# Performance work log

Hardware: AMD Instinct MI355X
Metric: run time of the kernel (lower is better)

The kernel has to match this reference:

```python
import jax, jax.numpy as jnp
import numpy as np

N_CELLS, C_N, K, D_N = 128, 256, 16, 64
G, HS, HM, HMOD, HEADS = 8, 128, 128, 64, 4


def setup_inputs() -> dict:
    key = jax.random.key(0)
    ks = list(jax.random.split(key, 12))
    rng = np.random.default_rng(0)
    # top-K neighbors per neuron within each cell, self excluded, sorted (as in __init__)
    scores = rng.random((N_CELLS, C_N, C_N), dtype=np.float32)
    scores[:, np.arange(C_N), np.arange(C_N)] = -np.inf
    topk = np.argpartition(-scores, K, axis=-1)[..., :K]
    conn_idx = jnp.asarray(np.sort(topk, axis=-1).astype(np.int32))
    cell_to_group = jnp.asarray((np.arange(N_CELLS) % G).astype(np.int32))

    def nrm(k, shape, scale):
        return jax.random.normal(k, shape, dtype=jnp.float32) * scale

    inp = {
        'h': nrm(ks[0], (N_CELLS, C_N, D_N), 1.0),
        'neuron_id': nrm(ks[1], (N_CELLS, C_N, D_N), 0.02),
        'neuron_key': nrm(ks[2], (N_CELLS, C_N, D_N), 0.02),
        'state_w1': nrm(ks[3], (HS, 2 * D_N), (2.0 / (2 * D_N)) ** 0.5),
        'state_b1': jnp.zeros((HS,), jnp.float32),
        'state_gs1': jnp.ones((G, HS), jnp.float32),
        'state_gb1': jnp.zeros((G, HS), jnp.float32),
        'state_w2': nrm(ks[4], (D_N, HS), 0.1 * (2.0 / HS) ** 0.5),
        'state_b2': jnp.zeros((D_N,), jnp.float32),
        'state_gs2': jnp.ones((G, D_N), jnp.float32),
        'state_gb2': jnp.zeros((G, D_N), jnp.float32),
        'msg_w1': nrm(ks[5], (HM, 2 * D_N), (2.0 / (2 * D_N)) ** 0.5),
        'msg_b1': jnp.zeros((HM,), jnp.float32),
        'msg_gs1': jnp.ones((G, HM), jnp.float32),
        'msg_gb1': jnp.zeros((G, HM), jnp.float32),
        'msg_w2': nrm(ks[6], (D_N, HM), 0.1 * (2.0 / HM) ** 0.5),
        'msg_b2': jnp.zeros((D_N,), jnp.float32),
        'msg_gs2': jnp.ones((G, D_N), jnp.float32),
        'msg_gb2': jnp.zeros((G, D_N), jnp.float32),
        'mod_w1': nrm(ks[7], (N_CELLS, D_N, HMOD), (2.0 / D_N) ** 0.5),
        'mod_b1': jnp.zeros((N_CELLS, HMOD), jnp.float32),
        'mod_w2': nrm(ks[8], (N_CELLS, HMOD, D_N), 0.01 * (2.0 / HMOD) ** 0.5),
        'mod_b2': jnp.zeros((N_CELLS, D_N), jnp.float32),
        'conn_idx': conn_idx,
        'cell_to_group': cell_to_group,
    }
    return inp


def reference(h, neuron_id, neuron_key,
              state_w1, state_b1, state_gs1, state_gb1,
              state_w2, state_b2, state_gs2, state_gb2,
              msg_w1, msg_b1, msg_gs1, msg_gb1,
              msg_w2, msg_b2, msg_gs2, msg_gb2,
              mod_w1, mod_b1, mod_w2, mod_b2,
              conn_idx, cell_to_group):
    g = cell_to_group  # [N]
    dh = D_N // HEADS
    gather = jax.vmap(lambda per_cell, idx: per_cell[idx])  # [C,D],[C,K] -> [C,K,D]

    nbr = gather(h, conn_idx)          # [N,C,K,D] neighbor states
    kid = gather(neuron_id, conn_idx)  # [N,C,K,D] neighbor identity vectors

    # multi-head attention weights over the K neighbors
    q = neuron_key.reshape(N_CELLS, C_N, HEADS, dh)
    kk = kid.reshape(N_CELLS, C_N, K, HEADS, dh)
    logits = jnp.einsum('nchd,nckhd->nckh', q, kk) / (dh ** 0.5)
    attn = jax.nn.softmax(logits, axis=2)  # softmax over K

    # per-edge message MLP with per-group gain/bias
    x = jnp.concatenate([nbr, jnp.broadcast_to(h[:, :, None, :], nbr.shape)], axis=-1)  # [N,C,K,2D]
    m1 = jax.nn.gelu(jnp.einsum('nckf,hf->nckh', x, msg_w1) + msg_b1)
    m1 = m1 * msg_gs1[g][:, None, None, :] + msg_gb1[g][:, None, None, :]
    m2 = jnp.einsum('nckh,dh->nckd', m1, msg_w2) + msg_b2
    m2 = m2 * msg_gs2[g][:, None, None, :] + msg_gb2[g][:, None, None, :]

    # attention-weighted aggregation over neighbors
    m2h = m2.reshape(N_CELLS, C_N, K, HEADS, dh)
    agg = jnp.einsum('nckh,nckhd->nchd', attn, m2h).reshape(N_CELLS, C_N, D_N)

    # state-update MLP with per-group gain/bias
    s_in = jnp.concatenate([h, agg], axis=-1)  # [N,C,2D]
    s1 = jax.nn.gelu(jnp.einsum('ncf,hf->nch', s_in, state_w1) + state_b1)
    s1 = s1 * state_gs1[g][:, None, :] + state_gb1[g][:, None, :]
    delta = jnp.einsum('nch,dh->ncd', s1, state_w2) + state_b2
    delta = delta * state_gs2[g][:, None, :] + state_gb2[g][:, None, :]

    # per-cell batched modulation MLP (mod_w1/mod_w2) gating the update
    pooled = h.mean(axis=1)  # [N,D]
    mh = jnp.tanh(jnp.einsum('nd,ndh->nh', pooled, mod_w1) + mod_b1)
    gate = jnp.tanh(jnp.einsum('nh,nho->no', mh, mod_w2) + mod_b2)  # [N,D]

    return h + gate[:, None, :] * delta
```

## Files before the change

kernel.cpp:

```cpp
#include <hip/hip_runtime.h>
#include <hip/hip_bf16.h>

#define N_CELLS 128
#define C_N     256
#define K_NB    16
#define D_N     64
#define G_N     8
#define HS      128
#define HM      128
#define HMOD    64

typedef __bf16 bf16x8 __attribute__((ext_vector_type(8)));
typedef float  f32x4v __attribute__((ext_vector_type(4)));


__device__ __forceinline__ float rl(float v, int l) {
    return __uint_as_float((unsigned)__builtin_amdgcn_readlane((int)__float_as_uint(v), l));
}

__device__ __forceinline__ unsigned cvtpk(float lo, float hi) {
    __hip_bfloat162 t = __float22bfloat162_rn(float2{lo, hi});
    return *reinterpret_cast<unsigned*>(&t);
}

__device__ __forceinline__ unsigned short f2bf(float f) {
    return (unsigned short)(cvtpk(f, 0.f) & 0xffffu);
}

__device__ __forceinline__ float bflo(unsigned u) { return __uint_as_float(u << 16); }
__device__ __forceinline__ float bfhi(unsigned u) { return __uint_as_float(u & 0xffff0000u); }

__device__ __forceinline__ f32x4v mfma16(uint4 a, uint4 b, f32x4v c) {
    return __builtin_amdgcn_mfma_f32_16x16x32_bf16(
        __builtin_bit_cast(bf16x8, a), __builtin_bit_cast(bf16x8, b), c, 0, 0, 0);
}

__device__ __forceinline__ float gelu_f(float x) {
    float x2 = x * x;
    float u  = x * fmaf(x2, 0.044715f, 1.0f);
    float e  = __expf(1.5957691216057308f * u);
    float r  = __builtin_amdgcn_rcpf(e + 1.0f);
    return x - x * r;
}

__device__ __forceinline__ float tanh_fast(float z) {
    float e = __expf(2.0f * z);
    return 1.0f - 2.0f / (e + 1.0f);
}

__device__ __forceinline__ uint4 packf8(const float* p) {
    float4 a = *(const float4*)p, b = *(const float4*)(p + 4);
    return make_uint4(cvtpk(a.x, a.y), cvtpk(a.z, a.w), cvtpk(b.x, b.y), cvtpk(b.z, b.w));
}

__device__ __forceinline__ void load_w2_folded(
    const float* __restrict__ w2, const float* __restrict__ gs1,
    const float* __restrict__ gb1, const float* __restrict__ gs2,
    const float* __restrict__ b2, const float* __restrict__ gb2,
    int g, int lrow, int lgrp, uint4 wf[4][4], float c2[4])
{
    #pragma unroll
    for (int nb2 = 0; nb2 < 4; ++nb2) {
        int d = nb2 * 16 + lrow;
        float gs2d = gs2[g * 64 + d];
        float cgb = 0.0f;
        #pragma unroll
        for (int kf = 0; kf < 4; ++kf) {
            int k0 = kf * 32 + lgrp * 8;
            const float* wp = w2 + d * 128 + k0;
            float4 wa = *(const float4*)wp, wb = *(const float4*)(wp + 4);
            const float* gp = gs1 + g * 128 + k0;
            float4 ga = *(const float4*)gp, gbv = *(const float4*)(gp + 4);
            const float* bp = gb1 + g * 128 + k0;
            float4 ba = *(const float4*)bp, bbv = *(const float4*)(bp + 4);
            cgb += wa.x*ba.x + wa.y*ba.y + wa.z*ba.z + wa.w*ba.w
                 + wb.x*bbv.x + wb.y*bbv.y + wb.z*bbv.z + wb.w*bbv.w;
            wf[nb2][kf] = make_uint4(
                cvtpk(wa.x*ga.x*gs2d,  wa.y*ga.y*gs2d),
                cvtpk(wa.z*ga.z*gs2d,  wa.w*ga.w*gs2d),
                cvtpk(wb.x*gbv.x*gs2d, wb.y*gbv.y*gs2d),
                cvtpk(wb.z*gbv.z*gs2d, wb.w*gbv.w*gs2d));
        }
        cgb += __shfl_xor(cgb, 16);
        cgb += __shfl_xor(cgb, 32);
        c2[nb2] = fmaf(gs2d, cgb + b2[d], gb2[g * 64 + d]);
    }
}


__global__ __launch_bounds__(1024) void gate_kernel(
    const float* __restrict__ h,
    const float* __restrict__ mod_w1, const float* __restrict__ mod_b1,
    const float* __restrict__ mod_w2, const float* __restrict__ mod_b2,
    float* __restrict__ gatep)
{
    __shared__ float red[16][64];
    __shared__ float pooled[64];
    __shared__ float mh[64];
    int n = blockIdx.x, tid = threadIdx.x;
    int d = tid & 63, part = tid >> 6;
    const float* hn = h + (size_t)n * C_N * 64;
    float acc = 0.0f;
    #pragma unroll 4
    for (int i = 0; i < 16; ++i) acc += hn[(part * 16 + i) * 64 + d];
    red[part][d] = acc;
    __syncthreads();
    if (tid < 64) {
        float s = 0.0f;
        #pragma unroll
        for (int p = 0; p < 16; ++p) s += red[p][d];
        pooled[d] = s * (1.0f / 256.0f);
    }
    __syncthreads();
    if (tid < 64) {
        float a1 = mod_b1[n * HMOD + d];
        for (int q = 0; q < 64; ++q)
            a1 = fmaf(pooled[q], mod_w1[((size_t)n * 64 + q) * HMOD + d], a1);
        mh[d] = tanh_fast(a1);
    }
    __syncthreads();
    if (tid < 64) {
        float a2 = mod_b2[n * 64 + d];
        for (int q = 0; q < HMOD; ++q)
            a2 = fmaf(mh[q], mod_w2[((size_t)n * HMOD + q) * 64 + d], a2);
        gatep[n * 64 + d] = tanh_fast(a2);
    }
}


__global__ __launch_bounds__(512, 4) void node_kernel(
    const float* __restrict__ h, const float* __restrict__ msg_w1,
    const float* __restrict__ msg_b1,
    unsigned short* __restrict__ yws, unsigned short* __restrict__ bews)
{
    __shared__ __align__(16) unsigned short ybuf_all[8][16 * 256];
    int tid = threadIdx.x, bid = blockIdx.x;
    int n = bid >> 1;
    int wave = tid >> 6, lane = tid & 63;
    int lrow = lane & 15, lgrp = lane >> 4;
    int c0 = (bid & 1) * 128 + wave * 16;
    unsigned short* ybuf = ybuf_all[wave];

    uint4 bf[2];
    {
        const float* hp = h + ((size_t)n * C_N + (c0 + lrow)) * 64;
        bf[0] = packf8(hp + lgrp * 8);
        bf[1] = packf8(hp + 32 + lgrp * 8);
    }
    for (int nbM = 0; nbM < 16; ++nbM) {
        int o = nbM * 16 + lrow;
        uint4 af[2];
        #pragma unroll
        for (int kf = 0; kf < 2; ++kf) {
            int k = kf * 32 + lgrp * 8;
            const float* wp = (o < 128) ? (msg_w1 + (size_t)o * 128 + k)
                                        : (msg_w1 + (size_t)(o - 128) * 128 + 64 + k);
            af[kf] = packf8(wp);
        }
        f32x4v acc = {0.f, 0.f, 0.f, 0.f};
        acc = mfma16(af[0], bf[0], acc);
        acc = mfma16(af[1], bf[1], acc);
        float4 addv = {0.f, 0.f, 0.f, 0.f};
        if (nbM >= 8) addv = *(const float4*)(msg_b1 + (nbM - 8) * 16 + lgrp * 4);
        uint2 pk = make_uint2(cvtpk(acc[0] + addv.x, acc[1] + addv.y),
                              cvtpk(acc[2] + addv.z, acc[3] + addv.w));
        int byte = lrow * 512 + ((nbM * 32 + lgrp * 8) ^ ((lrow & 7) << 4));
        *reinterpret_cast<uint2*>(reinterpret_cast<char*>(ybuf) + byte) = pk;
    }
    #pragma unroll
    for (int pass = 0; pass < 8; ++pass) {
        int idx = pass * 64 + lane;
        int row = idx >> 5, col = idx & 31;
        int byte = row * 512 + ((col * 16) ^ ((row & 7) << 4));
        uint4 v = *reinterpret_cast<const uint4*>(reinterpret_cast<const char*>(ybuf) + byte);
        size_t rb = (((size_t)n * C_N + c0 + row) * 128) * 2;
        if (col < 16)
            *reinterpret_cast<uint4*>(reinterpret_cast<char*>(yws) + rb + col * 16) = v;
        else
            *reinterpret_cast<uint4*>(reinterpret_cast<char*>(bews) + rb + (col - 16) * 16) = v;
    }
}


__global__ __launch_bounds__(256, 4) void att_kernel(
    const float* __restrict__ neuron_id, const float* __restrict__ neuron_key,
    const int* __restrict__ conn_idx, float* __restrict__ attw)
{
    int tid = threadIdx.x, bid = blockIdx.x;
    int wave = tid >> 6, lane = tid & 63;
    int lrow = lane & 15, t = lane >> 4;
    int base = bid * 64 + wave * 16;

    for (int i = 0; i < 16; ++i) {
        int gidx = base + i;
        int jv = conn_idx[(size_t)gidx * 16 + lrow];
        const float* kp = neuron_id + ((size_t)(gidx & ~255) + jv) * 64 + t * 16;
        const float* qp = neuron_key + (size_t)gidx * 64 + t * 16;
        float4 k0 = *(const float4*)kp,       k1 = *(const float4*)(kp + 4),
               k2 = *(const float4*)(kp + 8), k3 = *(const float4*)(kp + 12);
        float4 q0 = *(const float4*)qp,       q1 = *(const float4*)(qp + 4),
               q2 = *(const float4*)(qp + 8), q3 = *(const float4*)(qp + 12);
        float dt = k0.x*q0.x + k0.y*q0.y + k0.z*q0.z + k0.w*q0.w
                 + k1.x*q1.x + k1.y*q1.y + k1.z*q1.z + k1.w*q1.w
                 + k2.x*q2.x + k2.y*q2.y + k2.z*q2.z + k2.w*q2.w
                 + k3.x*q3.x + k3.y*q3.y + k3.z*q3.z + k3.w*q3.w;
        float lg = dt * 0.25f;
        float mx = lg;
        mx = fmaxf(mx, __shfl_xor(mx, 1));
        mx = fmaxf(mx, __shfl_xor(mx, 2));
        mx = fmaxf(mx, __shfl_xor(mx, 4));
        mx = fmaxf(mx, __shfl_xor(mx, 8));
        float ex = __expf(lg - mx);
        float sm = ex;
        sm += __shfl_xor(sm, 1);
        sm += __shfl_xor(sm, 2);
        sm += __shfl_xor(sm, 4);
        sm += __shfl_xor(sm, 8);
        attw[(size_t)gidx * 64 + lane] = ex * __builtin_amdgcn_rcpf(sm);
    }
}


__global__ __launch_bounds__(256, 4) void edge_kernel(
    const unsigned short* __restrict__ yws, const unsigned short* __restrict__ bews,
    const float* __restrict__ attw, const int* __restrict__ conn_idx,
    const float* __restrict__ msg_w2, const float* __restrict__ msg_gs1,
    const float* __restrict__ msg_gb1, const float* __restrict__ msg_gs2,
    const float* __restrict__ msg_b2, const float* __restrict__ msg_gb2,
    const int* __restrict__ cell_to_group,
    unsigned short* __restrict__ aggws)
{
    __shared__ __align__(16) unsigned short pbuf_all[4][4 * 8 * 128];
    __shared__ __align__(16) unsigned short aggT_all[4][8 * 64];
    int tid = threadIdx.x, bid = blockIdx.x;
    int wave = tid >> 6, lane = tid & 63;
    int lrow = lane & 15, lgrp = lane >> 4;
    int base = bid * 32 + wave * 8;
    int n = base >> 8;
    unsigned short* pbuf = pbuf_all[wave];
    unsigned short* aggT = aggT_all[wave];
    const char* ycell = (const char*)yws + (size_t)n * C_N * 256;

    for (int ci = 0; ci < 8; ++ci) {
        int gidx = base + ci;
        float attreg = attw[(size_t)gidx * 64 + lane];
        unsigned bep = *reinterpret_cast<const unsigned*>(
            (const char*)bews + (size_t)gidx * 256 + lane * 4);
        float be0 = bflo(bep), be1 = bfhi(bep);
        int jv = conn_idx[(size_t)gidx * 16 + lrow];
        unsigned uy[16];
        #pragma unroll
        for (int k = 0; k < 16; ++k) {
            int j = __builtin_amdgcn_readlane(jv, k);
            uy[k] = *reinterpret_cast<const unsigned*>(ycell + (size_t)j * 256 + lane * 4);
        }
        float p0 = 0.f, p1 = 0.f, p2 = 0.f, p3 = 0.f,
              p4 = 0.f, p5 = 0.f, p6 = 0.f, p7 = 0.f;
        #pragma unroll
        for (int k = 0; k < 16; ++k) {
            float g0 = gelu_f(bflo(uy[k]) + be0);
            float g1 = gelu_f(bfhi(uy[k]) + be1);
            float a0 = rl(attreg, k),      a1 = rl(attreg, 16 + k);
            float a2 = rl(attreg, 32 + k), a3 = rl(attreg, 48 + k);
            p0 = fmaf(a0, g0, p0); p1 = fmaf(a0, g1, p1);
            p2 = fmaf(a1, g0, p2); p3 = fmaf(a1, g1, p3);
            p4 = fmaf(a2, g0, p4); p5 = fmaf(a2, g1, p5);
            p6 = fmaf(a3, g0, p6); p7 = fmaf(a3, g1, p7);
        }
        unsigned pk0 = cvtpk(p0, p1), pk1 = cvtpk(p2, p3),
                 pk2 = cvtpk(p4, p5), pk3 = cvtpk(p6, p7);
        int swz = (lane * 4) ^ ((ci & 7) << 4);
        char* pb = reinterpret_cast<char*>(pbuf);
        *reinterpret_cast<unsigned*>(pb + (0 * 8 + ci) * 256 + swz) = pk0;
        *reinterpret_cast<unsigned*>(pb + (1 * 8 + ci) * 256 + swz) = pk1;
        *reinterpret_cast<unsigned*>(pb + (2 * 8 + ci) * 256 + swz) = pk2;
        *reinterpret_cast<unsigned*>(pb + (3 * 8 + ci) * 256 + swz) = pk3;
    }

    uint4 w2f[4][4];
    float mb2c[4];
    int g = cell_to_group[n];
    load_w2_folded(msg_w2, msg_gs1, msg_gb1, msg_gs2, msg_b2, msg_gb2,
                   g, lrow, lgrp, w2f, mb2c);

    int arow = lrow & 7;
    #pragma unroll
    for (int t = 0; t < 4; ++t) {
        f32x4v acc = {0.f, 0.f, 0.f, 0.f};
        #pragma unroll
        for (int kf = 0; kf < 4; ++kf) {
            uint4 a = *reinterpret_cast<const uint4*>(
                reinterpret_cast<const char*>(pbuf) +
                (t * 8 + arow) * 256 + ((kf * 64 + lgrp * 16) ^ (arow << 4)));
            acc = mfma16(a, w2f[t][kf], acc);
        }
        if (lgrp < 2) {
            #pragma unroll
            for (int r = 0; r < 4; ++r) {
                float v = acc[r] + mb2c[t];
                int c = lgrp * 4 + r;
                int byte = c * 128 + ((((t * 16 + lrow)) * 2) ^ ((c & 7) << 4));
                *reinterpret_cast<unsigned short*>(reinterpret_cast<char*>(aggT) + byte) = f2bf(v);
            }
        }
    }
    {
        int row = lane >> 3, col = lane & 7;
        int byte = row * 128 + ((col * 16) ^ ((row & 7) << 4));
        uint4 v = *reinterpret_cast<const uint4*>(reinterpret_cast<const char*>(aggT) + byte);
        *reinterpret_cast<uint4*>((char*)aggws + (size_t)(base + row) * 128 + col * 16) = v;
    }
}


__global__ __launch_bounds__(512, 4) void state_kernel(
    const float* __restrict__ h, const unsigned short* __restrict__ aggws,
    const float* __restrict__ gatep,
    const float* __restrict__ state_w1, const float* __restrict__ state_b1,
    const float* __restrict__ state_gs1, const float* __restrict__ state_gb1,
    const float* __restrict__ state_w2, const float* __restrict__ state_b2,
    const float* __restrict__ state_gs2, const float* __restrict__ state_gb2,
    const int* __restrict__ cell_to_group, float* __restrict__ out)
{
    __shared__ __align__(16) unsigned short w1s[128 * 128];
    __shared__ __align__(16) unsigned short s1b_all[8][16 * 128];
    int tid = threadIdx.x, bid = blockIdx.x;
    int n = bid >> 1;
    int g = cell_to_group[n];

    for (int idx = tid; idx < 2048; idx += 512) {
        int row = idx >> 4, ch = idx & 15;
        uint4 p = packf8(state_w1 + (size_t)row * 128 + ch * 8);
        int byte = row * 256 + ((ch * 16) ^ ((row & 7) << 4));
        *reinterpret_cast<uint4*>(reinterpret_cast<char*>(w1s) + byte) = p;
    }
    __syncthreads();

    int wave = tid >> 6, lane = tid & 63;
    int lrow = lane & 15, lgrp = lane >> 4;
    int c0 = (bid & 1) * 128 + wave * 16;
    unsigned short* s1b = s1b_all[wave];

    uint4 sB[4];
    {
        const float* hp = h + ((size_t)n * C_N + c0 + lrow) * 64;
        sB[0] = packf8(hp + lgrp * 8);
        sB[1] = packf8(hp + 32 + lgrp * 8);
        const char* ap = (const char*)aggws + ((size_t)n * C_N + c0 + lrow) * 128;
        sB[2] = *reinterpret_cast<const uint4*>(ap + lgrp * 16);
        sB[3] = *reinterpret_cast<const uint4*>(ap + 64 + lgrp * 16);
    }
    for (int nbM = 0; nbM < 8; ++nbM) {
        uint4 wA[4];
        #pragma unroll
        for (int kf = 0; kf < 4; ++kf)
            wA[kf] = *reinterpret_cast<const uint4*>(
                reinterpret_cast<const char*>(w1s) +
                (nbM * 16 + lrow) * 256 + ((kf * 64 + lgrp * 16) ^ ((lrow & 7) << 4)));
        f32x4v acc = {0.f, 0.f, 0.f, 0.f};
        #pragma unroll
        for (int kf = 0; kf < 4; ++kf) acc = mfma16(wA[kf], sB[kf], acc);
        float4 b1q = *(const float4*)(state_b1 + nbM * 16 + lgrp * 4);
        float g0 = gelu_f(acc[0] + b1q.x), g1 = gelu_f(acc[1] + b1q.y);
        float g2 = gelu_f(acc[2] + b1q.z), g3 = gelu_f(acc[3] + b1q.w);
        uint2 pk = make_uint2(cvtpk(g0, g1), cvtpk(g2, g3));
        int byte = lrow * 256 + ((nbM * 32 + lgrp * 8) ^ ((lrow & 7) << 4));
        *reinterpret_cast<uint2*>(reinterpret_cast<char*>(s1b) + byte) = pk;
    }

    uint4 w2sf[4][4];
    float sb2c[4];
    load_w2_folded(state_w2, state_gs1, state_gb1, state_gs2, state_b2, state_gb2,
                   g, lrow, lgrp, w2sf, sb2c);
    uint4 s1A[4];
    #pragma unroll
    for (int kf = 0; kf < 4; ++kf)
        s1A[kf] = *reinterpret_cast<const uint4*>(
            reinterpret_cast<const char*>(s1b) +
            lrow * 256 + ((kf * 64 + lgrp * 16) ^ ((lrow & 7) << 4)));

    float* dT = reinterpret_cast<float*>(s1b);
    #pragma unroll
    for (int nb2 = 0; nb2 < 4; ++nb2) {
        f32x4v acc = {0.f, 0.f, 0.f, 0.f};
        #pragma unroll
        for (int kf = 0; kf < 4; ++kf) acc = mfma16(s1A[kf], w2sf[nb2][kf], acc);
        #pragma unroll
        for (int r = 0; r < 4; ++r) {
            int c = lgrp * 4 + r;
            int d = nb2 * 16 + lrow;
            int byte = c * 256 + ((d * 4) ^ ((c & 7) << 4));
            *reinterpret_cast<float*>(reinterpret_cast<char*>(dT) + byte) = acc[r] + sb2c[nb2];
        }
    }
    #pragma unroll
    for (int pass = 0; pass < 4; ++pass) {
        int idx = pass * 64 + lane;
        int row = idx >> 4, col = idx & 15;
        int byte = row * 256 + ((col * 16) ^ ((row & 7) << 4));
        float4 dv = *reinterpret_cast<const float4*>(reinterpret_cast<const char*>(dT) + byte);
        size_t off = ((size_t)n * C_N + c0 + row) * 64 + col * 4;
        float4 hv = *(const float4*)(h + off);
        float4 gv = *(const float4*)(gatep + n * 64 + col * 4);
        float4 o;
        o.x = fmaf(gv.x, dv.x, hv.x);
        o.y = fmaf(gv.y, dv.y, hv.y);
        o.z = fmaf(gv.z, dv.z, hv.z);
        o.w = fmaf(gv.w, dv.w, hv.w);
        *(float4*)(out + off) = o;
    }
}


extern "C" void kernel_launch(void* const* d_in, const int* in_sizes, int n_in,
                              void* d_out, int out_size, void* d_ws, size_t ws_size,
                              hipStream_t stream) {
    (void)in_sizes; (void)n_in; (void)out_size; (void)ws_size;
    const float* h          = (const float*)d_in[0];
    const float* neuron_id  = (const float*)d_in[1];
    const float* neuron_key = (const float*)d_in[2];
    const float* state_w1   = (const float*)d_in[3];
    const float* state_b1   = (const float*)d_in[4];
    const float* state_gs1  = (const float*)d_in[5];
    const float* state_gb1  = (const float*)d_in[6];
    const float* state_w2   = (const float*)d_in[7];
    const float* state_b2   = (const float*)d_in[8];
    const float* state_gs2  = (const float*)d_in[9];
    const float* state_gb2  = (const float*)d_in[10];
    const float* msg_w1     = (const float*)d_in[11];
    const float* msg_b1     = (const float*)d_in[12];
    const float* msg_gs1    = (const float*)d_in[13];
    const float* msg_gb1    = (const float*)d_in[14];
    const float* msg_w2     = (const float*)d_in[15];
    const float* msg_b2     = (const float*)d_in[16];
    const float* msg_gs2    = (const float*)d_in[17];
    const float* msg_gb2    = (const float*)d_in[18];
    const float* mod_w1     = (const float*)d_in[19];
    const float* mod_b1     = (const float*)d_in[20];
    const float* mod_w2     = (const float*)d_in[21];
    const float* mod_b2     = (const float*)d_in[22];
    const int*   conn_idx   = (const int*)d_in[23];
    const int*   c2g        = (const int*)d_in[24];

    char* ws = (char*)d_ws;
    float*          gatep = (float*)ws;
    unsigned short* yws   = (unsigned short*)(ws + (32u << 10));
    unsigned short* bews  = (unsigned short*)(ws + (32u << 10) + (8u << 20));
    float*          attws = (float*)(ws + (32u << 10) + (16u << 20));
    unsigned short* aggws = (unsigned short*)(ws + (32u << 10) + (24u << 20));
    float* outp = (float*)d_out;

    gate_kernel<<<dim3(N_CELLS), dim3(1024), 0, stream>>>(
        h, mod_w1, mod_b1, mod_w2, mod_b2, gatep);
    node_kernel<<<dim3(256), dim3(512), 0, stream>>>(
        h, msg_w1, msg_b1, yws, bews);
    att_kernel<<<dim3(512), dim3(256), 0, stream>>>(
        neuron_id, neuron_key, conn_idx, attws);
    edge_kernel<<<dim3(1024), dim3(256), 0, stream>>>(
        yws, bews, attws, conn_idx,
        msg_w2, msg_gs1, msg_gb1, msg_gs2, msg_b2, msg_gb2, c2g, aggws);
    state_kernel<<<dim3(256), dim3(512), 0, stream>>>(
        h, aggws, gatep,
        state_w1, state_b1, state_gs1, state_gb1,
        state_w2, state_b2, state_gs2, state_gb2, c2g, outp);
}
```

Measured before the change: 130.5 us.

## Stage per-cell node projections in LDS for edge gathers and regroup blocks

The edge kernel now launches one 1024-thread block per half cell. Each block first copies that cell's whole 64 KB bf16 y slab into shared memory, so the 16 neighbor gathers per neuron read LDS instead of scattered global/L2 loads. The MFMA stage is restructured to run on batches of 4 neurons per wave, twice, using smaller per-wave buffers. In exchange, each cell's slab is loaded twice (once per half block), LDS use per block is large, and 4 waves of each MFMA tile are partly wasted, which limits occupancy.

```diff
diff --git a/kernel.cpp b/kernel.cpp
--- a/kernel.cpp
+++ b/kernel.cpp
@@ -221,7 +221,7 @@
 }
 
 
-__global__ __launch_bounds__(256, 4) void edge_kernel(
+__global__ __launch_bounds__(1024, 4) void edge_kernel(
     const unsigned short* __restrict__ yws, const unsigned short* __restrict__ bews,
     const float* __restrict__ attw, const int* __restrict__ conn_idx,
     const float* __restrict__ msg_w2, const float* __restrict__ msg_gs1,
@@ -230,85 +230,97 @@
     const int* __restrict__ cell_to_group,
     unsigned short* __restrict__ aggws)
 {
-    __shared__ __align__(16) unsigned short pbuf_all[4][4 * 8 * 128];
-    __shared__ __align__(16) unsigned short aggT_all[4][8 * 64];
+    __shared__ __align__(16) unsigned yl32[C_N * 64];
+    __shared__ __align__(16) unsigned short pbuf_all[16][16 * 128];
+    __shared__ __align__(16) unsigned short aggT_all[16][4 * 64];
     int tid = threadIdx.x, bid = blockIdx.x;
+    int n = bid >> 1;
+    int g = cell_to_group[n];
     int wave = tid >> 6, lane = tid & 63;
     int lrow = lane & 15, lgrp = lane >> 4;
-    int base = bid * 32 + wave * 8;
-    int n = base >> 8;
-    unsigned short* pbuf = pbuf_all[wave];
-    unsigned short* aggT = aggT_all[wave];
-    const char* ycell = (const char*)yws + (size_t)n * C_N * 256;
-
-    for (int ci = 0; ci < 8; ++ci) {
-        int gidx = base + ci;
-        float attreg = attw[(size_t)gidx * 64 + lane];
-        unsigned bep = *reinterpret_cast<const unsigned*>(
-            (const char*)bews + (size_t)gidx * 256 + lane * 4);
-        float be0 = bflo(bep), be1 = bfhi(bep);
-        int jv = conn_idx[(size_t)gidx * 16 + lrow];
-        unsigned uy[16];
-        #pragma unroll
-        for (int k = 0; k < 16; ++k) {
-            int j = __builtin_amdgcn_readlane(jv, k);
-            uy[k] = *reinterpret_cast<const unsigned*>(ycell + (size_t)j * 256 + lane * 4);
-        }
-        float p0 = 0.f, p1 = 0.f, p2 = 0.f, p3 = 0.f,
-              p4 = 0.f, p5 = 0.f, p6 = 0.f, p7 = 0.f;
-        #pragma unroll
-        for (int k = 0; k < 16; ++k) {
-            float g0 = gelu_f(bflo(uy[k]) + be0);
-            float g1 = gelu_f(bfhi(uy[k]) + be1);
-            float a0 = rl(attreg, k),      a1 = rl(attreg, 16 + k);
-            float a2 = rl(attreg, 32 + k), a3 = rl(attreg, 48 + k);
-            p0 = fmaf(a0, g0, p0); p1 = fmaf(a0, g1, p1);
-            p2 = fmaf(a1, g0, p2); p3 = fmaf(a1, g1, p3);
-            p4 = fmaf(a2, g0, p4); p5 = fmaf(a2, g1, p5);
-            p6 = fmaf(a3, g0, p6); p7 = fmaf(a3, g1, p7);
-        }
-        unsigned pk0 = cvtpk(p0, p1), pk1 = cvtpk(p2, p3),
-                 pk2 = cvtpk(p4, p5), pk3 = cvtpk(p6, p7);
-        int swz = (lane * 4) ^ ((ci & 7) << 4);
-        char* pb = reinterpret_cast<char*>(pbuf);
-        *reinterpret_cast<unsigned*>(pb + (0 * 8 + ci) * 256 + swz) = pk0;
-        *reinterpret_cast<unsigned*>(pb + (1 * 8 + ci) * 256 + swz) = pk1;
-        *reinterpret_cast<unsigned*>(pb + (2 * 8 + ci) * 256 + swz) = pk2;
-        *reinterpret_cast<unsigned*>(pb + (3 * 8 + ci) * 256 + swz) = pk3;
+    int base = n * C_N + (bid & 1) * 128 + wave * 8;
+
+    {
+        const uint4* src = (const uint4*)((const char*)yws + (size_t)n * C_N * 256);
+        uint4* dst = (uint4*)yl32;
+        #pragma unroll
+        for (int it = 0; it < 4; ++it) dst[it * 1024 + tid] = src[it * 1024 + tid];
     }
 
     uint4 w2f[4][4];
     float mb2c[4];
-    int g = cell_to_group[n];
     load_w2_folded(msg_w2, msg_gs1, msg_gb1, msg_gs2, msg_b2, msg_gb2,
                    g, lrow, lgrp, w2f, mb2c);
-
-    int arow = lrow & 7;
-    #pragma unroll
-    for (int t = 0; t < 4; ++t) {
-        f32x4v acc = {0.f, 0.f, 0.f, 0.f};
-        #pragma unroll
-        for (int kf = 0; kf < 4; ++kf) {
-            uint4 a = *reinterpret_cast<const uint4*>(
-                reinterpret_cast<const char*>(pbuf) +
-                (t * 8 + arow) * 256 + ((kf * 64 + lgrp * 16) ^ (arow << 4)));
-            acc = mfma16(a, w2f[t][kf], acc);
-        }
-        if (lgrp < 2) {
+    __syncthreads();
+
+    char* pbuf_b = reinterpret_cast<char*>(pbuf_all[wave]);
+    char* aggT_b = reinterpret_cast<char*>(aggT_all[wave]);
+    const unsigned* bews32 = (const unsigned*)bews;
+
+    #pragma unroll 1
+    for (int batch = 0; batch < 2; ++batch) {
+        #pragma unroll 1
+        for (int cis = 0; cis < 4; ++cis) {
+            int gidx = base + batch * 4 + cis;
+            float attreg = attw[(size_t)gidx * 64 + lane];
+            unsigned bep = bews32[(size_t)gidx * 64 + lane];
+            float be0 = bflo(bep), be1 = bfhi(bep);
+            int jv = conn_idx[(size_t)gidx * 16 + lrow];
+            unsigned uy[16];
             #pragma unroll
-            for (int r = 0; r < 4; ++r) {
-                float v = acc[r] + mb2c[t];
-                int c = lgrp * 4 + r;
-                int byte = c * 128 + ((((t * 16 + lrow)) * 2) ^ ((c & 7) << 4));
-                *reinterpret_cast<unsigned short*>(reinterpret_cast<char*>(aggT) + byte) = f2bf(v);
+            for (int k = 0; k < 16; ++k) {
+                int j = __builtin_amdgcn_readlane(jv, k);
+                uy[k] = yl32[j * 64 + lane];
             }
-        }
-    }
-    {
-        int row = lane >> 3, col = lane & 7;
-        int byte = row * 128 + ((col * 16) ^ ((row & 7) << 4));
-        uint4 v = *reinterpret_cast<const uint4*>(reinterpret_cast<const char*>(aggT) + byte);
-        *reinterpret_cast<uint4*>((char*)aggws + (size_t)(base + row) * 128 + col * 16) = v;
+            float p0 = 0.f, p1 = 0.f, p2 = 0.f, p3 = 0.f,
+                  p4 = 0.f, p5 = 0.f, p6 = 0.f, p7 = 0.f;
+            #pragma unroll
+            for (int k = 0; k < 16; ++k) {
+                float g0 = gelu_f(bflo(uy[k]) + be0);
+                float g1 = gelu_f(bfhi(uy[k]) + be1);
+                float a0 = rl(attreg, k),      a1 = rl(attreg, 16 + k);
+                float a2 = rl(attreg, 32 + k), a3 = rl(attreg, 48 + k);
+                p0 = fmaf(a0, g0, p0); p1 = fmaf(a0, g1, p1);
+                p2 = fmaf(a1, g0, p2); p3 = fmaf(a1, g1, p3);
+                p4 = fmaf(a2, g0, p4); p5 = fmaf(a2, g1, p5);
+                p6 = fmaf(a3, g0, p6); p7 = fmaf(a3, g1, p7);
+            }
+            unsigned pk0 = cvtpk(p0, p1), pk1 = cvtpk(p2, p3),
+                     pk2 = cvtpk(p4, p5), pk3 = cvtpk(p6, p7);
+            #pragma unroll
+            for (int t = 0; t < 4; ++t) {
+                unsigned pk = (t == 0) ? pk0 : (t == 1) ? pk1 : (t == 2) ? pk2 : pk3;
+                int row = t * 4 + cis;
+                int byte = row * 256 + ((lane * 4) ^ ((row & 7) << 4));
+                *reinterpret_cast<unsigned*>(pbuf_b + byte) = pk;
+            }
+        }
+        #pragma unroll
+        for (int t = 0; t < 4; ++t) {
+            f32x4v acc = {0.f, 0.f, 0.f, 0.f};
+            #pragma unroll
+            for (int kf = 0; kf < 4; ++kf) {
+                int row = t * 4 + (lrow & 3);
+                uint4 a = *reinterpret_cast<const uint4*>(
+                    pbuf_b + row * 256 + ((kf * 64 + lgrp * 16) ^ ((row & 7) << 4)));
+                acc = mfma16(a, w2f[t][kf], acc);
+            }
+            if (lgrp == 0) {
+                #pragma unroll
+                for (int r = 0; r < 4; ++r) {
+                    float v = acc[r] + mb2c[t];
+                    int byte = r * 128 + ((((t * 16 + lrow)) * 2) ^ ((r & 7) << 4));
+                    *reinterpret_cast<unsigned short*>(aggT_b + byte) = f2bf(v);
+                }
+            }
+        }
+        if (lane < 32) {
+            int row = lane >> 3, col = lane & 7;
+            int byte = row * 128 + ((col * 16) ^ ((row & 7) << 4));
+            uint4 v = *reinterpret_cast<const uint4*>(aggT_b + byte);
+            *reinterpret_cast<uint4*>(
+                (char*)aggws + (size_t)(base + batch * 4 + row) * 128 + col * 16) = v;
+        }
     }
 }
 
@@ -456,7 +468,7 @@
         h, msg_w1, msg_b1, yws, bews);
     att_kernel<<<dim3(512), dim3(256), 0, stream>>>(
         neuron_id, neuron_key, conn_idx, attws);
-    edge_kernel<<<dim3(1024), dim3(256), 0, stream>>>(
+    edge_kernel<<<dim3(256), dim3(1024), 0, stream>>>(
         yws, bews, attws, conn_idx,
         msg_w2, msg_gs1, msg_gb1, msg_gs2, msg_b2, msg_gb2, c2g, aggws);
     state_kernel<<<dim3(256), dim3(512), 0, stream>>>(
```

Measured after the change: 132.2 us. No clear change (+1.3%).
